# Performance work log

Measured on AMD Instinct MI355X. Metric: run time of the kernel, lower is better.

Reference implementation:

```python
import jax, jax.numpy as jnp
import numpy as np

B, C, H, Wd = 16, 512, 56, 56
WCH = 128  # W_ch: projection rank of phi/rou


def setup_inputs() -> dict:
    key = jax.random.key(0)
    ks = jax.random.split(key, 8)
    s = 0.02
    return {
        "x": jax.random.normal(ks[0], (B, C, H, Wd), dtype=jnp.float32),
        "y": jax.random.normal(ks[1], (B, C, H, Wd), dtype=jnp.float32),
        # phi: Conv2d(C, WCH, 1) -> weight [WCH, C], bias [WCH]
        "phi_w": jax.random.normal(ks[2], (WCH, C), dtype=jnp.float32) * s,
        "phi_b": jnp.zeros((WCH,), dtype=jnp.float32),
        # rou: Conv2d(C, WCH, 1) applied to globally pooled y -> acts as Linear
        "rou_w": jax.random.normal(ks[3], (WCH, C), dtype=jnp.float32) * s,
        "rou_b": jnp.zeros((WCH,), dtype=jnp.float32),
        # zeta: Linear(C, C)
        "zeta_w": jax.random.normal(ks[4], (C, C), dtype=jnp.float32) * s,
        "zeta_b": jnp.zeros((C,), dtype=jnp.float32),
    }


def reference(x, y, phi_w, phi_b, rou_w, rou_b, zeta_w, zeta_b):
    b, c, h, w = x.shape
    hw = h * w
    # phi_xT = relu(phi(x)).view(B, WCH, HW); phi_x = transpose -> [B, HW, WCH]
    phi_xT = jax.nn.relu(jnp.einsum('kc,bchw->bkhw', phi_w, x) + phi_b[None, :, None, None])
    phi_x = phi_xT.reshape(b, -1, hw).transpose(0, 2, 1)  # [B, HW, WCH]
    # rou_y = sigmoid(rou(global_avg_pool(y))) -> [B, WCH]
    pooled = y.mean(axis=(2, 3))  # [B, C]
    rou_y = jax.nn.sigmoid(pooled @ rou_w.T + rou_b)  # [B, WCH]
    # D_i = sum_j (phi_x diag(rou) phi_x^T)_{ij} = sum_k phi_x[i,k] rou[k] s[k]
    s = phi_x.sum(axis=1)  # [B, WCH], column sums
    D = jnp.einsum('bnk,bk,bk->bn', phi_x, rou_y, s)  # [B, HW]
    inv_sqrt = 1.0 / jnp.sqrt(D + 1e-8)
    P = phi_x * inv_sqrt[..., None]  # diag(D^-1/2) @ phi_x, [B, HW, WCH]
    # x.view(B, -1, C): raw row-major reshape of [B,C,H,W] (NOT a transpose)
    x_trans = x.reshape(b, hw, c)
    # LX = x_trans - P diag(rou) P^T x_trans, re-associated right-to-left
    t = jnp.einsum('bnk,bnc->bkc', P, x_trans)          # P^T x_trans, [B, WCH, C]
    LX = x_trans - jnp.einsum('bnk,bk,bkc->bnc', P, rou_y, t)
    # zeta Linear + dropout(eval: identity) + relu, residual add
    out = jax.nn.relu(LX @ zeta_w.T + zeta_b)
    return x + out.reshape(b, c, h, w)
```

## Files before the change

kernel.cpp:

```cpp
#include <hip/hip_runtime.h>
#include <math.h>

#define B_  16
#define C_  512
#define HW_ 3136
#define K_  128
#define CHW (C_ * HW_)

typedef __bf16 bf16x8_t __attribute__((ext_vector_type(8)));
typedef __bf16 bf16x4_t __attribute__((ext_vector_type(4)));
typedef __bf16 bf16x2_t __attribute__((ext_vector_type(2)));
typedef float floatx4  __attribute__((ext_vector_type(4)));

typedef const __attribute__((address_space(1))) void* gas_ptr;
typedef __attribute__((address_space(3))) void*       las_ptr;

static __device__ __forceinline__ unsigned short bfbits(__bf16 v) {
    return __builtin_bit_cast(unsigned short, v);
}

__device__ __forceinline__ void stage128x64(const __bf16* __restrict__ base, long ld,
                                            int row0, int rowmax, int k0,
                                            __bf16* lds, int t) {
    int w = t >> 6;
    #pragma unroll
    for (int i = 0; i < 4; ++i) {
        int u = i * 256 + t;
        int m = u >> 3, slot = u & 7;
        int kg = slot ^ (m & 7);
        int r = row0 + m; if (r > rowmax) r = rowmax;
        const __bf16* g = base + (long)r * ld + (k0 + kg * 8);
        __bf16* l = lds + (size_t)(i * 256 + w * 64) * 8;
        __builtin_amdgcn_global_load_lds((gas_ptr)g, (las_ptr)l, 16, 0, 0);
    }
}

__device__ __forceinline__ void stage_tr_phi(const __bf16* __restrict__ src,
                                             int n0, int p0, char* Bs, int t) {
    int ng = t & 15;
    int cp2 = (t >> 4) * 2;
    #pragma unroll
    for (int ci = 0; ci < 2; ++ci) {
        int cc = cp2 + ci * 32;
        const __bf16* g0 = src + (long)(p0 + cc) * HW_ + n0 + ng * 8;
        bf16x8_t v0 = *(const bf16x8_t*)g0;
        bf16x8_t v1 = *(const bf16x8_t*)(g0 + HW_);
        int r8 = cc >> 3, sub = (cc & 7) >> 1;
        #pragma unroll
        for (int j = 0; j < 8; ++j) {
            int row = ng * 8 + j;
            int slot = (r8 + row + (row >> 3)) & 7;
            unsigned int pr = ((unsigned int)bfbits(v1[j]) << 16) | bfbits(v0[j]);
            *(unsigned int*)(Bs + row * 144 + slot * 16 + sub * 4) = pr;
        }
    }
}

__device__ __forceinline__ void stage_tr_t(const __bf16* __restrict__ src,
                                           const float* __restrict__ isrc,
                                           int c0, int p0, char* Bs, int t) {
    int cg = t & 15;
    int np2 = (t >> 4) * 2;
    #pragma unroll
    for (int ni = 0; ni < 2; ++ni) {
        int nn = np2 + ni * 32;
        int n = p0 + nn;
        float s0 = isrc[n], s1 = isrc[n + 1];
        const __bf16* g0 = src + (long)n * C_ + c0 + cg * 8;
        bf16x8_t v0 = *(const bf16x8_t*)g0;
        bf16x8_t v1 = *(const bf16x8_t*)(g0 + C_);
        int r8 = nn >> 3, sub = (nn & 7) >> 1;
        #pragma unroll
        for (int j = 0; j < 8; ++j) {
            int row = cg * 8 + j;
            int slot = (r8 + row + (row >> 3)) & 7;
            __bf16 a0 = (__bf16)((float)v0[j] * s0);
            __bf16 a1 = (__bf16)((float)v1[j] * s1);
            unsigned int pr = ((unsigned int)bfbits(a1) << 16) | bfbits(a0);
            *(unsigned int*)(Bs + row * 144 + slot * 16 + sub * 4) = pr;
        }
    }
}

__device__ __forceinline__ void mma_step64(const char* As, const char* Bs,
                                           floatx4 acc[4][4], int aoff, int boff,
                                           int q, int lxor) {
    #pragma unroll
    for (int h = 0; h < 2; ++h) {
        int s = (((h * 4 + q) ^ lxor) << 4);
        bf16x8_t af[4], bf[4];
        #pragma unroll
        for (int i = 0; i < 4; ++i) af[i] = *(const bf16x8_t*)(As + aoff + i * 2048 + s);
        #pragma unroll
        for (int i = 0; i < 4; ++i) bf[i] = *(const bf16x8_t*)(Bs + boff + i * 2048 + s);
        #pragma unroll
        for (int mi = 0; mi < 4; ++mi)
            #pragma unroll
            for (int ni = 0; ni < 4; ++ni)
                acc[mi][ni] = __builtin_amdgcn_mfma_f32_16x16x32_bf16(af[mi], bf[ni], acc[mi][ni], 0, 0, 0);
    }
}

__device__ __forceinline__ void mma_step_mix(const char* As, const char* Bs,
                                             floatx4 acc[4][4], int lm, int q,
                                             int wrow, int wcol) {
    int lxor = lm & 7;
    int aoff = (wrow * 64 + lm) * 128;
    #pragma unroll
    for (int h = 0; h < 2; ++h) {
        int g = h * 4 + q;
        int sa = (g ^ lxor) << 4;
        bf16x8_t af[4], bf[4];
        #pragma unroll
        for (int i = 0; i < 4; ++i) af[i] = *(const bf16x8_t*)(As + aoff + i * 2048 + sa);
        #pragma unroll
        for (int i = 0; i < 4; ++i) {
            int brow = wcol * 64 + i * 16 + lm;
            int slot = (g + brow + (brow >> 3)) & 7;
            bf[i] = *(const bf16x8_t*)(Bs + brow * 144 + slot * 16);
        }
        #pragma unroll
        for (int mi = 0; mi < 4; ++mi)
            #pragma unroll
            for (int ni = 0; ni < 4; ++ni)
                acc[mi][ni] = __builtin_amdgcn_mfma_f32_16x16x32_bf16(af[mi], bf[ni], acc[mi][ni], 0, 0, 0);
    }
}


__global__ __launch_bounds__(256) void k_pool(const float* __restrict__ y,
                                              float* __restrict__ pooled) {
    int bc = blockIdx.x;
    const float* yp = y + (long)bc * HW_;
    int t = threadIdx.x;
    float acc = 0.f;
    #pragma unroll
    for (int i = 0; i < 4; ++i) {
        int n4 = t + i * 256;
        if (n4 < 784) {
            float4 v = *reinterpret_cast<const float4*>(yp + (long)n4 * 4);
            acc += v.x + v.y + v.z + v.w;
        }
    }
    #pragma unroll
    for (int off = 32; off > 0; off >>= 1) acc += __shfl_xor(acc, off, 64);
    __shared__ float red[4];
    if ((t & 63) == 0) red[t >> 6] = acc;
    __syncthreads();
    if (t == 0) pooled[bc] = (red[0] + red[1] + red[2] + red[3]) * (1.0f / HW_);
}

__global__ __launch_bounds__(64) void k_rou(const float* __restrict__ pooled,
                                            const float* __restrict__ rou_w,
                                            const float* __restrict__ rou_b,
                                            float* __restrict__ rou_y) {
    int k = blockIdx.x;
    int b = blockIdx.y;
    int lane = threadIdx.x;
    const float* pr = pooled + b * C_;
    const float* wr = rou_w + (long)k * C_;
    float acc = 0.f;
    #pragma unroll
    for (int i = 0; i < 2; ++i) {
        int c = (lane + i * 64) * 4;
        float4 w4 = *reinterpret_cast<const float4*>(wr + c);
        float4 p4 = *reinterpret_cast<const float4*>(pr + c);
        acc += w4.x * p4.x + w4.y * p4.y + w4.z * p4.z + w4.w * p4.w;
    }
    #pragma unroll
    for (int off = 32; off > 0; off >>= 1) acc += __shfl_xor(acc, off, 64);
    if (lane == 0) rou_y[b * K_ + k] = 1.0f / (1.0f + expf(-(acc + rou_b[k])));
}

__global__ __launch_bounds__(256) void k_cast8(const float* __restrict__ a,
                                               __bf16* __restrict__ o) {
    long i = ((long)blockIdx.x * 256 + threadIdx.x) * 8;
    float4 v0 = *reinterpret_cast<const float4*>(a + i);
    float4 v1 = *reinterpret_cast<const float4*>(a + i + 4);
    bf16x8_t r;
    r[0] = (__bf16)v0.x; r[1] = (__bf16)v0.y; r[2] = (__bf16)v0.z; r[3] = (__bf16)v0.w;
    r[4] = (__bf16)v1.x; r[5] = (__bf16)v1.y; r[6] = (__bf16)v1.z; r[7] = (__bf16)v1.w;
    *reinterpret_cast<bf16x8_t*>(o + i) = r;
}


__global__ __launch_bounds__(256) void k_phi_m(const __bf16* __restrict__ xbf2,
                                               const __bf16* __restrict__ pwbf,
                                               const float* __restrict__ phi_b,
                                               __bf16* __restrict__ phi_kn,
                                               __bf16* __restrict__ phi_nk,
                                               float* __restrict__ sbuf) {
    int b = blockIdx.y;
    int n0 = blockIdx.x * 128;
    __shared__ __attribute__((aligned(16))) char smem[2 * 34816];
    int t = threadIdx.x, w = t >> 6, lane = t & 63;
    int lm = lane & 15, q = lane >> 4;
    int wrow = w >> 1, wcol = w & 1;
    floatx4 acc[4][4];
    #pragma unroll
    for (int i = 0; i < 4; ++i)
        #pragma unroll
        for (int j = 0; j < 4; ++j) acc[i][j] = (floatx4){0.f, 0.f, 0.f, 0.f};

    const __bf16* Bb = xbf2 + (long)b * CHW;

    stage128x64(pwbf, C_, 0, K_ - 1, 0, (__bf16*)smem, t);
    stage_tr_phi(Bb, n0, 0, smem + 16384, t);
    __syncthreads();
    int cur = 0;
    #pragma unroll
    for (int s = 0; s < 8; ++s) {
        char* cb = smem + cur * 34816;
        if (s < 7) {
            char* nb = smem + (cur ^ 1) * 34816;
            int p0 = (s + 1) * 64;
            stage128x64(pwbf, C_, 0, K_ - 1, p0, (__bf16*)nb, t);
            stage_tr_phi(Bb, n0, p0, nb + 16384, t);
        }
        mma_step_mix(cb, cb + 16384, acc, lm, q, wrow, wcol);
        __syncthreads();
        cur ^= 1;
    }
    #pragma unroll
    for (int mi = 0; mi < 4; ++mi) {
        int kb = wrow * 64 + mi * 16 + q * 4;
        float4 pb = *reinterpret_cast<const float4*>(phi_b + kb);
        float pbv[4] = {pb.x, pb.y, pb.z, pb.w};
        float sv[4] = {0.f, 0.f, 0.f, 0.f};
        #pragma unroll
        for (int ni = 0; ni < 4; ++ni) {
            int n = n0 + wcol * 64 + ni * 16 + lm;
            if (n < HW_) {
                bf16x4_t pack;
                #pragma unroll
                for (int r = 0; r < 4; ++r) {
                    float v = fmaxf(acc[mi][ni][r] + pbv[r], 0.f);
                    __bf16 vb = (__bf16)v;
                    phi_kn[((long)b * K_ + kb + r) * HW_ + n] = vb;
                    pack[r] = vb;
                    sv[r] += v;
                }
                *reinterpret_cast<bf16x4_t*>(phi_nk + ((long)b * HW_ + n) * K_ + kb) = pack;
            }
        }
        #pragma unroll
        for (int r = 0; r < 4; ++r) {
            float v = sv[r];
            v += __shfl_xor(v, 1, 64); v += __shfl_xor(v, 2, 64);
            v += __shfl_xor(v, 4, 64); v += __shfl_xor(v, 8, 64);
            if (lm == 0) atomicAdd(&sbuf[b * K_ + kb + r], v);
        }
    }
}

__global__ __launch_bounds__(256) void k_d2(__bf16* __restrict__ phi_nk,
                                            const float* __restrict__ rou_y,
                                            const float* __restrict__ s,
                                            float* __restrict__ inv_s) {
    int b = blockIdx.y;
    __shared__ float ws[K_];
    int t = threadIdx.x;
    if (t < K_) ws[t] = rou_y[b * K_ + t] * s[b * K_ + t];
    __syncthreads();
    int w = t >> 6, lane = t & 63;
    int n = blockIdx.x * 4 + w;
    __bf16* p = phi_nk + ((long)b * HW_ + n) * K_ + lane * 2;
    bf16x2_t v = *reinterpret_cast<bf16x2_t*>(p);
    float f0 = (float)v[0], f1 = (float)v[1];
    float d = f0 * ws[lane * 2] + f1 * ws[lane * 2 + 1];
    #pragma unroll
    for (int off = 32; off > 0; off >>= 1) d += __shfl_xor(d, off, 64);
    float inv = rsqrtf(d + 1e-8f);
    bf16x2_t o; o[0] = (__bf16)(f0 * inv); o[1] = (__bf16)(f1 * inv);
    *reinterpret_cast<bf16x2_t*>(p) = o;
    if (lane == 0) inv_s[b * HW_ + n] = inv;
}

__global__ __launch_bounds__(256) void k_t_m(const __bf16* __restrict__ phi_kn,
                                             const __bf16* __restrict__ xbf2,
                                             const float* __restrict__ inv_s,
                                             float* __restrict__ t_part) {
    int gid = blockIdx.x;
    int rlo = gid & 7, cc4 = (gid >> 3) & 3, r8 = gid >> 5;
    int r = r8 * 8 + rlo;
    int b = r / 7, nch = r % 7;
    int c0 = cc4 * 128;
    __shared__ __attribute__((aligned(16))) char smem[2 * 34816];
    int t = threadIdx.x, w = t >> 6, lane = t & 63;
    int lm = lane & 15, q = lane >> 4;
    int wrow = w >> 1, wcol = w & 1;
    floatx4 acc[4][4];
    #pragma unroll
    for (int i = 0; i < 4; ++i)
        #pragma unroll
        for (int j = 0; j < 4; ++j) acc[i][j] = (floatx4){0.f, 0.f, 0.f, 0.f};

    const __bf16* Ab = phi_kn + (long)b * K_ * HW_;
    const __bf16* Bb = xbf2 + (long)b * CHW;
    const float* ib = inv_s + (long)b * HW_;

    int pstart = nch * 448;
    stage128x64(Ab, HW_, 0, K_ - 1, pstart, (__bf16*)smem, t);
    stage_tr_t(Bb, ib, c0, pstart, smem + 16384, t);
    __syncthreads();
    int cur = 0;
    #pragma unroll
    for (int s = 0; s < 7; ++s) {
        char* cb = smem + cur * 34816;
        if (s < 6) {
            char* nb = smem + (cur ^ 1) * 34816;
            int p0 = pstart + (s + 1) * 64;
            stage128x64(Ab, HW_, 0, K_ - 1, p0, (__bf16*)nb, t);
            stage_tr_t(Bb, ib, c0, p0, nb + 16384, t);
        }
        mma_step_mix(cb, cb + 16384, acc, lm, q, wrow, wcol);
        __syncthreads();
        cur ^= 1;
    }
    float* outp = t_part + ((long)nch * B_ + b) * K_ * C_;
    #pragma unroll
    for (int mi = 0; mi < 4; ++mi) {
        int kb = wrow * 64 + mi * 16 + q * 4;
        #pragma unroll
        for (int ni = 0; ni < 4; ++ni) {
            int c = c0 + wcol * 64 + ni * 16 + lm;
            #pragma unroll
            for (int rr = 0; rr < 4; ++rr)
                outp[(long)(kb + rr) * C_ + c] = acc[mi][ni][rr];
        }
    }
}

__global__ __launch_bounds__(256) void k_tred(const float* __restrict__ t_part,
                                              __bf16* __restrict__ t_bf) {
    const long BKC = (long)B_ * K_ * C_;
    long i = ((long)blockIdx.x * 256 + threadIdx.x) * 4;
    float4 s = *reinterpret_cast<const float4*>(t_part + i);
    #pragma unroll
    for (int p = 1; p < 7; ++p) {
        float4 v = *reinterpret_cast<const float4*>(t_part + p * BKC + i);
        s.x += v.x; s.y += v.y; s.z += v.z; s.w += v.w;
    }
    bf16x4_t o;
    o[0] = (__bf16)s.x; o[1] = (__bf16)s.y; o[2] = (__bf16)s.z; o[3] = (__bf16)s.w;
    *reinterpret_cast<bf16x4_t*>(t_bf + i) = o;
}

__global__ __launch_bounds__(256) void k_tz_m(const __bf16* __restrict__ zwbf,
                                              const __bf16* __restrict__ t_bf,
                                              const float* __restrict__ rou_y,
                                              __bf16* __restrict__ tzT) {
    int b = blockIdx.y;
    int c0 = blockIdx.x * 128;
    __shared__ __attribute__((aligned(16))) char smem[2 * 32768];
    int t = threadIdx.x, w = t >> 6, lane = t & 63;
    int lm = lane & 15, q = lane >> 4;
    int wrow = w >> 1, wcol = w & 1;
    floatx4 acc[4][4];
    #pragma unroll
    for (int i = 0; i < 4; ++i)
        #pragma unroll
        for (int j = 0; j < 4; ++j) acc[i][j] = (floatx4){0.f, 0.f, 0.f, 0.f};

    const __bf16* Bb = t_bf + (long)b * K_ * C_;
    int lxor = lm & 7;
    int aoff = (wrow * 64 + lm) * 128;
    int boff = (wcol * 64 + lm) * 128;

    stage128x64(zwbf, C_, c0, C_ - 1, 0, (__bf16*)smem, t);
    stage128x64(Bb,   C_, 0, K_ - 1, 0, (__bf16*)(smem + 16384), t);
    __syncthreads();
    int cur = 0;
    #pragma unroll
    for (int s = 0; s < 8; ++s) {
        char* cb = smem + cur * 32768;
        if (s < 7) {
            char* nb = smem + (cur ^ 1) * 32768;
            int p0 = (s + 1) * 64;
            stage128x64(zwbf, C_, c0, C_ - 1, p0, (__bf16*)nb, t);
            stage128x64(Bb,   C_, 0, K_ - 1, p0, (__bf16*)(nb + 16384), t);
        }
        mma_step64(cb, cb + 16384, acc, aoff, boff, q, lxor);
        __syncthreads();
        cur ^= 1;
    }
    #pragma unroll
    for (int mi = 0; mi < 4; ++mi) {
        int c = c0 + wrow * 64 + mi * 16 + q * 4;
        #pragma unroll
        for (int ni = 0; ni < 4; ++ni) {
            int k = wcol * 64 + ni * 16 + lm;
            float rk = rou_y[b * K_ + k];
            #pragma unroll
            for (int rr = 0; rr < 4; ++rr)
                tzT[((long)b * C_ + c + rr) * K_ + k] = (__bf16)(-rk * acc[mi][ni][rr]);
        }
    }
}

__global__ __launch_bounds__(256) void k_out_m(const __bf16* __restrict__ xbf2,
                                               const __bf16* __restrict__ zwbf,
                                               const __bf16* __restrict__ pnk,
                                               const __bf16* __restrict__ tzT,
                                               const float* __restrict__ zeta_b,
                                               float* __restrict__ out) {
    int gid = blockIdx.x;
    int rlo = gid & 7, cc4 = (gid >> 3) & 3, r8 = gid >> 5;
    int r = r8 * 8 + rlo;
    int b = r / 25, nt = r % 25;
    int n0 = nt * 128;
    int c0 = cc4 * 128;
    __shared__ __attribute__((aligned(16))) char smem[2 * 32768];
    int t = threadIdx.x, w = t >> 6, lane = t & 63;
    int lm = lane & 15, q = lane >> 4;
    int wrow = w >> 1, wcol = w & 1;
    floatx4 acc[4][4];
    #pragma unroll
    for (int i = 0; i < 4; ++i)
        #pragma unroll
        for (int j = 0; j < 4; ++j) acc[i][j] = (floatx4){0.f, 0.f, 0.f, 0.f};

    int lxor = lm & 7;
    int aoff = (wrow * 64 + lm) * 128;
    int boff = (wcol * 64 + lm) * 128;

    const __bf16* A1 = xbf2 + (long)b * CHW;
    const __bf16* A2 = pnk + (long)b * (long)HW_ * K_;
    const __bf16* B2 = tzT + (long)b * (long)C_ * K_;

    stage128x64(A1,   C_, n0, HW_ - 1, 0, (__bf16*)smem, t);
    stage128x64(zwbf, C_, c0, C_ - 1, 0, (__bf16*)(smem + 16384), t);
    __syncthreads();
    int cur = 0;
    #pragma unroll
    for (int s = 0; s < 10; ++s) {
        char* cb = smem + cur * 32768;
        if (s < 9) {
            char* nb = smem + (cur ^ 1) * 32768;
            int sn = s + 1;
            if (sn < 8) {
                int p0 = sn * 64;
                stage128x64(A1,   C_, n0, HW_ - 1, p0, (__bf16*)nb, t);
                stage128x64(zwbf, C_, c0, C_ - 1, p0, (__bf16*)(nb + 16384), t);
            } else {
                int p0 = (sn - 8) * 64;
                stage128x64(A2, K_, n0, HW_ - 1, p0, (__bf16*)nb, t);
                stage128x64(B2, K_, c0, C_ - 1, p0, (__bf16*)(nb + 16384), t);
            }
        }
        mma_step64(cb, cb + 16384, acc, aoff, boff, q, lxor);
        __syncthreads();
        cur ^= 1;
    }
    float* ep = (float*)smem;
    const __bf16* xres = xbf2 + (long)b * CHW;
    int lr = t >> 3, lc = (t & 7) * 16;
    #pragma unroll
    for (int ch = 0; ch < 4; ++ch) {
        __syncthreads();
        if (wrow == (ch >> 1)) {
            #pragma unroll
            for (int mm = 0; mm < 2; ++mm) {
                int mi = (ch & 1) * 2 + mm;
                #pragma unroll
                for (int ni = 0; ni < 4; ++ni)
                    #pragma unroll
                    for (int rr = 0; rr < 4; ++rr)
                        ep[(mm * 16 + q * 4 + rr) * 132 + wcol * 64 + ni * 16 + lm] = acc[mi][ni][rr];
            }
        }
        __syncthreads();
        int n = n0 + ch * 32 + lr;
        if (n < HW_) {
            long rowbase = (long)n * C_ + c0 + lc;
            bf16x8_t x0 = *(const bf16x8_t*)(xres + rowbase);
            bf16x8_t x1 = *(const bf16x8_t*)(xres + rowbase + 8);
            float xv[16];
            #pragma unroll
            for (int j = 0; j < 8; ++j) { xv[j] = (float)x0[j]; xv[8 + j] = (float)x1[j]; }
            float* orow = out + (long)b * CHW + rowbase;
            #pragma unroll
            for (int jj = 0; jj < 4; ++jj) {
                float4 zb = *reinterpret_cast<const float4*>(zeta_b + c0 + lc + jj * 4);
                float4 e  = *reinterpret_cast<const float4*>(&ep[lr * 132 + lc + jj * 4]);
                float4 o;
                o.x = xv[jj * 4 + 0] + fmaxf(e.x + zb.x, 0.f);
                o.y = xv[jj * 4 + 1] + fmaxf(e.y + zb.y, 0.f);
                o.z = xv[jj * 4 + 2] + fmaxf(e.z + zb.z, 0.f);
                o.w = xv[jj * 4 + 3] + fmaxf(e.w + zb.w, 0.f);
                *reinterpret_cast<float4*>(orow + jj * 4) = o;
            }
        }
    }
}

extern "C" void kernel_launch(void* const* d_in, const int* in_sizes, int n_in,
                              void* d_out, int out_size, void* d_ws, size_t ws_size,
                              hipStream_t stream) {
    const float* x      = (const float*)d_in[0];
    const float* y      = (const float*)d_in[1];
    const float* phi_w  = (const float*)d_in[2];
    const float* phi_b  = (const float*)d_in[3];
    const float* rou_w  = (const float*)d_in[4];
    const float* rou_b  = (const float*)d_in[5];
    const float* zeta_w = (const float*)d_in[6];
    const float* zeta_b = (const float*)d_in[7];
    float* out = (float*)d_out;

    char* p = (char*)d_ws;
    __bf16* xbf2   = (__bf16*)p; p += (size_t)B_ * CHW * 2;
    __bf16* phi_kn = (__bf16*)p; p += (size_t)B_ * K_ * HW_ * 2;
    __bf16* phi_nk = (__bf16*)p; p += (size_t)B_ * K_ * HW_ * 2;
    float*  t_part = (float*) p; p += (size_t)7 * B_ * K_ * C_ * 4;
    __bf16* t_bf   = (__bf16*)p; p += (size_t)B_ * K_ * C_ * 2;
    __bf16* tzT    = (__bf16*)p; p += (size_t)B_ * C_ * K_ * 2;
    __bf16* pwbf   = (__bf16*)p; p += (size_t)K_ * C_ * 2;
    __bf16* zwbf   = (__bf16*)p; p += (size_t)C_ * C_ * 2;
    float*  pooled = (float*) p; p += (size_t)B_ * C_ * 4;
    float*  rou_y  = (float*) p; p += (size_t)B_ * K_ * 4;
    float*  sbuf   = (float*) p; p += (size_t)B_ * K_ * 4;
    float*  inv_s  = (float*) p; p += (size_t)B_ * HW_ * 4;

    hipMemsetAsync(sbuf, 0, B_ * K_ * sizeof(float), stream);

    k_pool <<<B_ * C_, 256, 0, stream>>>(y, pooled);
    k_rou  <<<dim3(K_, B_), 64, 0, stream>>>(pooled, rou_w, rou_b, rou_y);
    k_cast8<<<(K_ * C_) / 2048, 256, 0, stream>>>(phi_w, pwbf);
    k_cast8<<<(C_ * C_) / 2048, 256, 0, stream>>>(zeta_w, zwbf);
    k_cast8<<<(B_ * (long)CHW) / 2048, 256, 0, stream>>>(x, xbf2);
    k_phi_m<<<dim3(25, B_), 256, 0, stream>>>(xbf2, pwbf, phi_b, phi_kn, phi_nk, sbuf);
    k_d2   <<<dim3(HW_ / 4, B_), 256, 0, stream>>>(phi_nk, rou_y, sbuf, inv_s);
    k_t_m  <<<448, 256, 0, stream>>>(phi_kn, xbf2, inv_s, t_part);
    k_tred <<<(B_ * K_ * C_) / 1024, 256, 0, stream>>>(t_part, t_bf);
    k_tz_m <<<dim3(C_ / 128, B_), 256, 0, stream>>>(zwbf, t_bf, rou_y, tzT);
    k_out_m<<<1600, 256, 0, stream>>>(xbf2, zwbf, phi_nk, tzT, zeta_b, out);
}
```

Before: 389.7 us.

## Vectorize D kernel, reduce split-K chunks, deepen prefetch in GEMM pipelines

k_d2 now handles 16 rows per block, loading 8 bf16 values per lane instead of 2 and reducing across 16 lanes. k_t_m splits the HW reduction into 4 chunks of 768 instead of 7 of 448, which shrinks the partial-sum buffer and the k_tred reduction but leaves only 256 blocks. k_tz_m and k_out_m move to a prefetch-two-ahead double-buffer scheme with explicit vmcnt/lgkmcnt waits and raw barriers, so global loads overlap more with MFMA work. The hand-placed waitcnt values depend on how many loads stage128x64 issues, so a wrong count could read stale shared memory.

```diff
diff --git a/kernel.cpp b/kernel.cpp
--- a/kernel.cpp
+++ b/kernel.cpp
@@ -263,17 +263,24 @@
     if (t < K_) ws[t] = rou_y[b * K_ + t] * s[b * K_ + t];
     __syncthreads();
     int w = t >> 6, lane = t & 63;
-    int n = blockIdx.x * 4 + w;
-    __bf16* p = phi_nk + ((long)b * HW_ + n) * K_ + lane * 2;
-    bf16x2_t v = *reinterpret_cast<bf16x2_t*>(p);
-    float f0 = (float)v[0], f1 = (float)v[1];
-    float d = f0 * ws[lane * 2] + f1 * ws[lane * 2 + 1];
-    #pragma unroll
-    for (int off = 32; off > 0; off >>= 1) d += __shfl_xor(d, off, 64);
+    int sub = lane >> 4, lm = lane & 15;
+    int n = blockIdx.x * 16 + w * 4 + sub;
+    __bf16* p = phi_nk + ((long)b * HW_ + n) * K_ + lm * 8;
+    bf16x8_t v = *reinterpret_cast<bf16x8_t*>(p);
+    float f[8];
+    #pragma unroll
+    for (int j = 0; j < 8; ++j) f[j] = (float)v[j];
+    float d = 0.f;
+    #pragma unroll
+    for (int j = 0; j < 8; ++j) d += f[j] * ws[lm * 8 + j];
+    d += __shfl_xor(d, 1, 64); d += __shfl_xor(d, 2, 64);
+    d += __shfl_xor(d, 4, 64); d += __shfl_xor(d, 8, 64);
     float inv = rsqrtf(d + 1e-8f);
-    bf16x2_t o; o[0] = (__bf16)(f0 * inv); o[1] = (__bf16)(f1 * inv);
-    *reinterpret_cast<bf16x2_t*>(p) = o;
-    if (lane == 0) inv_s[b * HW_ + n] = inv;
+    bf16x8_t o;
+    #pragma unroll
+    for (int j = 0; j < 8; ++j) o[j] = (__bf16)(f[j] * inv);
+    *reinterpret_cast<bf16x8_t*>(p) = o;
+    if (lm == 0) inv_s[b * HW_ + n] = inv;
 }
 
 __global__ __launch_bounds__(256) void k_t_m(const __bf16* __restrict__ phi_kn,
@@ -283,7 +290,7 @@
     int gid = blockIdx.x;
     int rlo = gid & 7, cc4 = (gid >> 3) & 3, r8 = gid >> 5;
     int r = r8 * 8 + rlo;
-    int b = r / 7, nch = r % 7;
+    int b = r >> 2, nch = r & 3;
     int c0 = cc4 * 128;
     __shared__ __attribute__((aligned(16))) char smem[2 * 34816];
     int t = threadIdx.x, w = t >> 6, lane = t & 63;
@@ -299,15 +306,15 @@
     const __bf16* Bb = xbf2 + (long)b * CHW;
     const float* ib = inv_s + (long)b * HW_;
 
-    int pstart = nch * 448;
+    int steps = (nch == 3) ? 13 : 12;
+    int pstart = nch * 768;
     stage128x64(Ab, HW_, 0, K_ - 1, pstart, (__bf16*)smem, t);
     stage_tr_t(Bb, ib, c0, pstart, smem + 16384, t);
     __syncthreads();
     int cur = 0;
-    #pragma unroll
-    for (int s = 0; s < 7; ++s) {
+    for (int s = 0; s < steps; ++s) {
         char* cb = smem + cur * 34816;
-        if (s < 6) {
+        if (s < steps - 1) {
             char* nb = smem + (cur ^ 1) * 34816;
             int p0 = pstart + (s + 1) * 64;
             stage128x64(Ab, HW_, 0, K_ - 1, p0, (__bf16*)nb, t);
@@ -337,7 +344,7 @@
     long i = ((long)blockIdx.x * 256 + threadIdx.x) * 4;
     float4 s = *reinterpret_cast<const float4*>(t_part + i);
     #pragma unroll
-    for (int p = 1; p < 7; ++p) {
+    for (int p = 1; p < 4; ++p) {
         float4 v = *reinterpret_cast<const float4*>(t_part + p * BKC + i);
         s.x += v.x; s.y += v.y; s.z += v.z; s.w += v.w;
     }
@@ -369,20 +376,27 @@
 
     stage128x64(zwbf, C_, c0, C_ - 1, 0, (__bf16*)smem, t);
     stage128x64(Bb,   C_, 0, K_ - 1, 0, (__bf16*)(smem + 16384), t);
-    __syncthreads();
-    int cur = 0;
+    {
+        char* b1 = smem + 32768;
+        stage128x64(zwbf, C_, c0, C_ - 1, 64, (__bf16*)b1, t);
+        stage128x64(Bb,   C_, 0, K_ - 1, 64, (__bf16*)(b1 + 16384), t);
+    }
     #pragma unroll
     for (int s = 0; s < 8; ++s) {
-        char* cb = smem + cur * 32768;
-        if (s < 7) {
-            char* nb = smem + (cur ^ 1) * 32768;
-            int p0 = (s + 1) * 64;
-            stage128x64(zwbf, C_, c0, C_ - 1, p0, (__bf16*)nb, t);
-            stage128x64(Bb,   C_, 0, K_ - 1, p0, (__bf16*)(nb + 16384), t);
-        }
+        char* cb = smem + (s & 1) * 32768;
+        if (s < 7) asm volatile("s_waitcnt vmcnt(8)" ::: "memory");
+        else       asm volatile("s_waitcnt vmcnt(0)" ::: "memory");
+        __builtin_amdgcn_s_barrier();
+        __builtin_amdgcn_sched_barrier(0);
         mma_step64(cb, cb + 16384, acc, aoff, boff, q, lxor);
-        __syncthreads();
-        cur ^= 1;
+        asm volatile("s_waitcnt lgkmcnt(0)" ::: "memory");
+        __builtin_amdgcn_s_barrier();
+        __builtin_amdgcn_sched_barrier(0);
+        if (s + 2 <= 7) {
+            int p0 = (s + 2) * 64;
+            stage128x64(zwbf, C_, c0, C_ - 1, p0, (__bf16*)cb, t);
+            stage128x64(Bb,   C_, 0, K_ - 1, p0, (__bf16*)(cb + 16384), t);
+        }
     }
     #pragma unroll
     for (int mi = 0; mi < 4; ++mi) {
@@ -428,30 +442,34 @@
     const __bf16* A2 = pnk + (long)b * (long)HW_ * K_;
     const __bf16* B2 = tzT + (long)b * (long)C_ * K_;
 
-    stage128x64(A1,   C_, n0, HW_ - 1, 0, (__bf16*)smem, t);
-    stage128x64(zwbf, C_, c0, C_ - 1, 0, (__bf16*)(smem + 16384), t);
-    __syncthreads();
-    int cur = 0;
+    #define OUT_STAGE(s_, buf_)                                                     \
+        do {                                                                        \
+            if ((s_) < 8) {                                                         \
+                stage128x64(A1,   C_, n0, HW_ - 1, (s_) * 64, (__bf16*)(buf_), t);  \
+                stage128x64(zwbf, C_, c0, C_ - 1,  (s_) * 64, (__bf16*)((buf_) + 16384), t); \
+            } else {                                                                \
+                stage128x64(A2, K_, n0, HW_ - 1, ((s_) - 8) * 64, (__bf16*)(buf_), t); \
+                stage128x64(B2, K_, c0, C_ - 1,  ((s_) - 8) * 64, (__bf16*)((buf_) + 16384), t); \
+            }                                                                       \
+        } while (0)
+
+    OUT_STAGE(0, smem);
+    OUT_STAGE(1, smem + 32768);
     #pragma unroll
     for (int s = 0; s < 10; ++s) {
-        char* cb = smem + cur * 32768;
-        if (s < 9) {
-            char* nb = smem + (cur ^ 1) * 32768;
-            int sn = s + 1;
-            if (sn < 8) {
-                int p0 = sn * 64;
-                stage128x64(A1,   C_, n0, HW_ - 1, p0, (__bf16*)nb, t);
-                stage128x64(zwbf, C_, c0, C_ - 1, p0, (__bf16*)(nb + 16384), t);
-            } else {
-                int p0 = (sn - 8) * 64;
-                stage128x64(A2, K_, n0, HW_ - 1, p0, (__bf16*)nb, t);
-                stage128x64(B2, K_, c0, C_ - 1, p0, (__bf16*)(nb + 16384), t);
-            }
-        }
+        char* cb = smem + (s & 1) * 32768;
+        if (s < 9) asm volatile("s_waitcnt vmcnt(8)" ::: "memory");
+        else       asm volatile("s_waitcnt vmcnt(0)" ::: "memory");
+        __builtin_amdgcn_s_barrier();
+        __builtin_amdgcn_sched_barrier(0);
         mma_step64(cb, cb + 16384, acc, aoff, boff, q, lxor);
-        __syncthreads();
-        cur ^= 1;
-    }
+        asm volatile("s_waitcnt lgkmcnt(0)" ::: "memory");
+        __builtin_amdgcn_s_barrier();
+        __builtin_amdgcn_sched_barrier(0);
+        if (s + 2 <= 9) OUT_STAGE(s + 2, cb);
+    }
+    #undef OUT_STAGE
+
     float* ep = (float*)smem;
     const __bf16* xres = xbf2 + (long)b * CHW;
     int lr = t >> 3, lc = (t & 7) * 16;
@@ -511,7 +529,7 @@
     __bf16* xbf2   = (__bf16*)p; p += (size_t)B_ * CHW * 2;
     __bf16* phi_kn = (__bf16*)p; p += (size_t)B_ * K_ * HW_ * 2;
     __bf16* phi_nk = (__bf16*)p; p += (size_t)B_ * K_ * HW_ * 2;
-    float*  t_part = (float*) p; p += (size_t)7 * B_ * K_ * C_ * 4;
+    float*  t_part = (float*) p; p += (size_t)4 * B_ * K_ * C_ * 4;
     __bf16* t_bf   = (__bf16*)p; p += (size_t)B_ * K_ * C_ * 2;
     __bf16* tzT    = (__bf16*)p; p += (size_t)B_ * C_ * K_ * 2;
     __bf16* pwbf   = (__bf16*)p; p += (size_t)K_ * C_ * 2;
@@ -529,8 +547,8 @@
     k_cast8<<<(C_ * C_) / 2048, 256, 0, stream>>>(zeta_w, zwbf);
     k_cast8<<<(B_ * (long)CHW) / 2048, 256, 0, stream>>>(x, xbf2);
     k_phi_m<<<dim3(25, B_), 256, 0, stream>>>(xbf2, pwbf, phi_b, phi_kn, phi_nk, sbuf);
-    k_d2   <<<dim3(HW_ / 4, B_), 256, 0, stream>>>(phi_nk, rou_y, sbuf, inv_s);
-    k_t_m  <<<448, 256, 0, stream>>>(phi_kn, xbf2, inv_s, t_part);
+    k_d2   <<<dim3(HW_ / 16, B_), 256, 0, stream>>>(phi_nk, rou_y, sbuf, inv_s);
+    k_t_m  <<<256, 256, 0, stream>>>(phi_kn, xbf2, inv_s, t_part);
     k_tred <<<(B_ * K_ * C_) / 1024, 256, 0, stream>>>(t_part, t_bf);
     k_tz_m <<<dim3(C_ / 128, B_), 256, 0, stream>>>(zwbf, t_bf, rou_y, tzT);
     k_out_m<<<1600, 256, 0, stream>>>(xbf2, zwbf, phi_nk, tzT, zeta_b, out);
```

Result: no change. 391.2 us (+0.4%).
